# Kernel tuning notes

Measured on AMD Instinct MI355X. Metric: run time of the kernel, lower is better.

The kernel has to match this reference:

```python
import jax, jax.numpy as jnp
import numpy as np

ALPHA = 0.25
GAMMA = 2.0
CONSTRAINT_WEIGHT = 2.0
EPOCH = 0  # current_epoch default


def _smooth_l1(s):
    # F.smooth_l1_loss(s, ones) elementwise, beta=1.0
    d = s - 1.0
    ad = jnp.abs(d)
    return jnp.where(ad < 1.0, 0.5 * d * d, ad - 0.5)


def setup_inputs() -> dict:
    key = jax.random.key(0)
    k1, k2 = jax.random.split(key)
    B = 131072
    outputs = jax.random.normal(k1, (B, 81, 9), dtype=jnp.float32)
    targets = jax.random.randint(k2, (B, 81), 0, 9, dtype=jnp.int64)
    return {"outputs": outputs, "targets": targets}


def reference(outputs, targets):
    B = outputs.shape[0]
    logits = outputs.reshape(B, 81, 9)
    logp = jax.nn.log_softmax(logits, axis=-1)          # [B,81,9]
    tgt = targets.reshape(B, 81)
    # per-cell cross entropy
    ce = -jnp.take_along_axis(logp, tgt[..., None], axis=-1)[..., 0]  # [B,81]
    pt = jnp.exp(-ce)
    focal_loss = jnp.mean(ALPHA * (1.0 - pt) ** GAMMA * ce)

    probs = jnp.exp(logp).reshape(B, 9, 9, 9)           # [B,row,col,digit]
    row_sums = probs.sum(axis=2)                        # [B,row,digit]
    col_sums = probs.sum(axis=1)                        # [B,col,digit]
    box_sums = probs.reshape(B, 3, 3, 3, 3, 9).sum(axis=(2, 4)).reshape(B, 9, 9)
    # sum over 9 digits of per-digit means == 9 * mean over all elements
    constraint_loss = 9.0 * (jnp.mean(_smooth_l1(row_sums))
                             + jnp.mean(_smooth_l1(col_sums))
                             + jnp.mean(_smooth_l1(box_sums)))
    constraint_loss = constraint_loss / 27.0

    epoch_factor = min(1.0, EPOCH / 50)
    dyn_w = CONSTRAINT_WEIGHT * (0.5 + 0.5 * epoch_factor)
    return focal_loss + dyn_w * constraint_loss
```

## Files before the change

kernel.cpp:

```cpp
#include <hip/hip_runtime.h>
#include <hip/hip_bf16.h>


constexpr int BLOCK = 256;
constexpr int WPB = 4;
constexpr float ALPHA = 0.25f;

__global__ __launch_bounds__(BLOCK) void focal_constraint_main(
    const float* __restrict__ outs,
    const int* __restrict__ tgts,
    double* __restrict__ acc,
    int ngroups)
{
    __shared__ float P[WPB * 729];
    __shared__ int   T[WPB * 81];
    __shared__ float red[WPB];

    const int lane = threadIdx.x & 63;
    const int wave = threadIdx.x >> 6;

    float lacc = 0.0f;

    for (int g = blockIdx.x; g < ngroups; g += gridDim.x) {
        const float4* __restrict__ src4 =
            reinterpret_cast<const float4*>(outs + (size_t)g * (WPB * 729));
        #pragma unroll
        for (int r = 0; r < 3; ++r) {
            const int idx = threadIdx.x + r * BLOCK;
            if (idx < 729) reinterpret_cast<float4*>(P)[idx] = src4[idx];
        }
        if (threadIdx.x < (WPB * 81) / 4) {
            reinterpret_cast<int4*>(T)[threadIdx.x] =
                reinterpret_cast<const int4*>(tgts + (size_t)g * (WPB * 81))[threadIdx.x];
        }
        __syncthreads();

        float* __restrict__ Ps = P + wave * 729;
        const int* __restrict__ Ts = T + wave * 81;
        #pragma unroll
        for (int cc = 0; cc < 2; ++cc) {
            const int cell = lane + cc * 64;
            if (cell < 81) {
                float v[9];
                #pragma unroll
                for (int d = 0; d < 9; ++d) v[d] = Ps[cell * 9 + d];
                float m = v[0];
                #pragma unroll
                for (int d = 1; d < 9; ++d) m = fmaxf(m, v[d]);
                float e[9];
                float sum = 0.0f;
                #pragma unroll
                for (int d = 0; d < 9; ++d) { e[d] = __expf(v[d] - m); sum += e[d]; }
                const float inv = 1.0f / sum;
                #pragma unroll
                for (int d = 0; d < 9; ++d) Ps[cell * 9 + d] = e[d] * inv;
                const int t = Ts[cell];
                const float ce = __logf(sum) - (v[t] - m);
                const float pt = e[t] * inv;
                const float om = 1.0f - pt;
                lacc += ALPHA * om * om * ce;
            }
        }
        __syncthreads();

        #pragma unroll
        for (int k = 0; k < 4; ++k) {
            const int idx = lane + k * 64;
            if (idx < 243) {
                const int grp = idx / 81;
                const int t2 = idx - grp * 81;
                const int a = t2 / 9;
                const int d = t2 - a * 9;
                float ssum = 0.0f;
                if (grp == 0) {
                    #pragma unroll
                    for (int c = 0; c < 9; ++c) ssum += Ps[(a * 9 + c) * 9 + d];
                } else if (grp == 1) {
                    #pragma unroll
                    for (int r = 0; r < 9; ++r) ssum += Ps[(r * 9 + a) * 9 + d];
                } else {
                    const int br = (a / 3) * 3, bc = (a % 3) * 3;
                    #pragma unroll
                    for (int i = 0; i < 3; ++i)
                        #pragma unroll
                        for (int j = 0; j < 3; ++j)
                            ssum += Ps[((br + i) * 9 + (bc + j)) * 9 + d];
                }
                const float dd = ssum - 1.0f;
                const float ad = fabsf(dd);
                const float sl1 = (ad < 1.0f) ? 0.5f * dd * dd : ad - 0.5f;
                lacc += sl1 * (1.0f / 3.0f);
            }
        }
        __syncthreads();
    }

    #pragma unroll
    for (int off = 32; off > 0; off >>= 1) lacc += __shfl_xor(lacc, off, 64);
    if (lane == 0) red[wave] = lacc;
    __syncthreads();
    if (threadIdx.x == 0) {
        double bsum = 0.0;
        #pragma unroll
        for (int w = 0; w < WPB; ++w) bsum += (double)red[w];
        atomicAdd(acc, bsum);
    }
}

__global__ void focal_constraint_finalize(const double* __restrict__ acc,
                                          float* __restrict__ out,
                                          double scale)
{
    out[0] = (float)(acc[0] * scale);
}

extern "C" void kernel_launch(void* const* d_in, const int* in_sizes, int n_in,
                              void* d_out, int out_size, void* d_ws, size_t ws_size,
                              hipStream_t stream) {
    const float* outs = (const float*)d_in[0];
    const int* tgts = (const int*)d_in[1];
    const int B = in_sizes[0] / 729;
    const int ngroups = B / WPB;

    double* acc = (double*)d_ws;
    hipMemsetAsync(acc, 0, sizeof(double), stream);

    int grid = 2048;
    if (grid > ngroups) grid = ngroups;
    focal_constraint_main<<<grid, BLOCK, 0, stream>>>(outs, tgts, acc, ngroups);

    const double scale = 1.0 / ((double)B * 81.0);
    focal_constraint_finalize<<<1, 1, 0, stream>>>(acc, (float*)d_out, scale);
}
```

Before: 533.8 us.

## Prefetch next group into registers and replace atomic with per-block partials

The main loop now issues nontemporal global loads for the next group into registers while the current group is processed out of shared memory, then stores them to LDS at the top of the next iteration. This software pipelining aims to hide global memory latency in a bandwidth-bound kernel. The global double atomicAdd and the memset are replaced by per-block partial sums that a 256-thread finalize kernel reduces. The cost is extra registers per thread and a slightly larger finalize kernel.

```diff
diff --git a/kernel.cpp b/kernel.cpp
--- a/kernel.cpp
+++ b/kernel.cpp
@@ -6,34 +6,61 @@
 constexpr int WPB = 4;
 constexpr float ALPHA = 0.25f;
 
+typedef float v4f __attribute__((ext_vector_type(4)));
+typedef int   v4i __attribute__((ext_vector_type(4)));
+
 __global__ __launch_bounds__(BLOCK) void focal_constraint_main(
     const float* __restrict__ outs,
     const int* __restrict__ tgts,
-    double* __restrict__ acc,
+    double* __restrict__ partials,
     int ngroups)
 {
     __shared__ float P[WPB * 729];
     __shared__ int   T[WPB * 81];
     __shared__ float red[WPB];
 
-    const int lane = threadIdx.x & 63;
-    const int wave = threadIdx.x >> 6;
+    const int tid = threadIdx.x;
+    const int lane = tid & 63;
+    const int wave = tid >> 6;
 
     float lacc = 0.0f;
 
-    for (int g = blockIdx.x; g < ngroups; g += gridDim.x) {
-        const float4* __restrict__ src4 =
-            reinterpret_cast<const float4*>(outs + (size_t)g * (WPB * 729));
-        #pragma unroll
-        for (int r = 0; r < 3; ++r) {
-            const int idx = threadIdx.x + r * BLOCK;
-            if (idx < 729) reinterpret_cast<float4*>(P)[idx] = src4[idx];
-        }
-        if (threadIdx.x < (WPB * 81) / 4) {
-            reinterpret_cast<int4*>(T)[threadIdx.x] =
-                reinterpret_cast<const int4*>(tgts + (size_t)g * (WPB * 81))[threadIdx.x];
+    int g = blockIdx.x;
+    v4f ra = {}, rb = {}, rc = {};
+    v4i rt = {};
+    {
+        const v4f* __restrict__ s4 =
+            reinterpret_cast<const v4f*>(outs + (size_t)g * (WPB * 729));
+        ra = __builtin_nontemporal_load(&s4[tid]);
+        rb = __builtin_nontemporal_load(&s4[tid + 256]);
+        if (tid < 729 - 512) rc = __builtin_nontemporal_load(&s4[tid + 512]);
+        const v4i* __restrict__ t4 =
+            reinterpret_cast<const v4i*>(tgts + (size_t)g * (WPB * 81));
+        if (tid < (WPB * 81) / 4) rt = __builtin_nontemporal_load(&t4[tid]);
+    }
+
+    for (; g < ngroups; g += gridDim.x) {
+        __syncthreads();
+        {
+            v4f* __restrict__ P4 = reinterpret_cast<v4f*>(P);
+            P4[tid] = ra;
+            P4[tid + 256] = rb;
+            if (tid < 729 - 512) P4[tid + 512] = rc;
+            if (tid < (WPB * 81) / 4) reinterpret_cast<v4i*>(T)[tid] = rt;
         }
         __syncthreads();
+
+        const int gn = g + gridDim.x;
+        if (gn < ngroups) {
+            const v4f* __restrict__ s4 =
+                reinterpret_cast<const v4f*>(outs + (size_t)gn * (WPB * 729));
+            ra = __builtin_nontemporal_load(&s4[tid]);
+            rb = __builtin_nontemporal_load(&s4[tid + 256]);
+            if (tid < 729 - 512) rc = __builtin_nontemporal_load(&s4[tid + 512]);
+            const v4i* __restrict__ t4 =
+                reinterpret_cast<const v4i*>(tgts + (size_t)gn * (WPB * 81));
+            if (tid < (WPB * 81) / 4) rt = __builtin_nontemporal_load(&t4[tid]);
+        }
 
         float* __restrict__ Ps = P + wave * 729;
         const int* __restrict__ Ts = T + wave * 81;
@@ -92,26 +119,36 @@
                 lacc += sl1 * (1.0f / 3.0f);
             }
         }
-        __syncthreads();
     }
 
     #pragma unroll
     for (int off = 32; off > 0; off >>= 1) lacc += __shfl_xor(lacc, off, 64);
     if (lane == 0) red[wave] = lacc;
     __syncthreads();
-    if (threadIdx.x == 0) {
+    if (tid == 0) {
         double bsum = 0.0;
         #pragma unroll
         for (int w = 0; w < WPB; ++w) bsum += (double)red[w];
-        atomicAdd(acc, bsum);
+        partials[blockIdx.x] = bsum;
     }
 }
 
-__global__ void focal_constraint_finalize(const double* __restrict__ acc,
-                                          float* __restrict__ out,
-                                          double scale)
+__global__ __launch_bounds__(256) void focal_constraint_finalize(
+    const double* __restrict__ partials,
+    float* __restrict__ out,
+    int n, double scale)
 {
-    out[0] = (float)(acc[0] * scale);
+    __shared__ double sred[4];
+    const int tid = threadIdx.x;
+    double s = 0.0;
+    for (int i = tid; i < n; i += 256) s += partials[i];
+    #pragma unroll
+    for (int off = 32; off > 0; off >>= 1) s += __shfl_xor(s, off, 64);
+    if ((tid & 63) == 0) sred[tid >> 6] = s;
+    __syncthreads();
+    if (tid == 0) {
+        out[0] = (float)((sred[0] + sred[1] + sred[2] + sred[3]) * scale);
+    }
 }
 
 extern "C" void kernel_launch(void* const* d_in, const int* in_sizes, int n_in,
@@ -122,13 +159,12 @@
     const int B = in_sizes[0] / 729;
     const int ngroups = B / WPB;
 
-    double* acc = (double*)d_ws;
-    hipMemsetAsync(acc, 0, sizeof(double), stream);
+    double* partials = (double*)d_ws;
 
     int grid = 2048;
     if (grid > ngroups) grid = ngroups;
-    focal_constraint_main<<<grid, BLOCK, 0, stream>>>(outs, tgts, acc, ngroups);
+    focal_constraint_main<<<grid, BLOCK, 0, stream>>>(outs, tgts, partials, ngroups);
 
     const double scale = 1.0 / ((double)B * 81.0);
-    focal_constraint_finalize<<<1, 1, 0, stream>>>(acc, (float*)d_out, scale);
+    focal_constraint_finalize<<<1, 256, 0, stream>>>(partials, (float*)d_out, grid, scale);
 }
```

Result: faster. 506.4 us (-5.1%).
